# Kernel tuning notes

Hardware: AMD Instinct MI355X
Metric: run time of the kernel (lower is better)

## Reference

```python
import jax, jax.numpy as jnp
import numpy as np

NUM_CLASSES = 81
THRESH_HI = 0.5
THRESH_LO = 0.4
GAMMA = 2.0
ALPHA = 0.25
VARIANCE = (0.1, 0.2)  # cfg['variance'] in ssd.pytorch
B, P, T = 32, 24564, 20


def setup_inputs() -> dict:
    key = jax.random.key(0)
    k1, k2, k3, k4, k5, k6, k7 = jax.random.split(key, 7)
    loc_data = jax.random.normal(k1, (B, P, 4), jnp.float32)
    conf_data = jax.random.normal(k2, (B, P, NUM_CLASSES), jnp.float32)
    # priors in center form (cx, cy, w, h), all in [0,1]
    pcxy = jax.random.uniform(k3, (P, 2), minval=0.05, maxval=0.95)
    pwh = jax.random.uniform(k4, (P, 2), minval=0.04, maxval=0.5)
    priors = jnp.concatenate([pcxy, pwh], axis=-1).astype(jnp.float32)
    # ground-truth boxes in point form (xmin, ymin, xmax, ymax) + label
    tcxy = jax.random.uniform(k5, (B, T, 2), minval=0.1, maxval=0.9)
    twh = jax.random.uniform(k6, (B, T, 2), minval=0.05, maxval=0.4)
    boxes = jnp.clip(jnp.concatenate([tcxy - twh / 2, tcxy + twh / 2], -1), 0.0, 1.0)
    labels = jax.random.randint(k7, (B, T), 0, NUM_CLASSES - 1).astype(jnp.float32)
    targets = jnp.concatenate([boxes, labels[..., None]], axis=-1)  # [B,T,5]
    return {"loc_data": loc_data, "conf_data": conf_data, "priors": priors, "targets": targets}


def point_form(pr):
    # center form -> (xmin,ymin,xmax,ymax)
    return jnp.concatenate([pr[:, :2] - pr[:, 2:] / 2, pr[:, :2] + pr[:, 2:] / 2], -1)


def jaccard(box_a, box_b):
    # box_a [T,4], box_b [P,4], both point form -> IoU [T,P]
    lt = jnp.maximum(box_a[:, None, :2], box_b[None, :, :2])
    rb = jnp.minimum(box_a[:, None, 2:], box_b[None, :, 2:])
    wh = jnp.clip(rb - lt, 0.0)
    inter = wh[..., 0] * wh[..., 1]
    area_a = ((box_a[:, 2] - box_a[:, 0]) * (box_a[:, 3] - box_a[:, 1]))[:, None]
    area_b = ((box_b[:, 2] - box_b[:, 0]) * (box_b[:, 3] - box_b[:, 1]))[None, :]
    return inter / (area_a + area_b - inter)


def encode(matched, priors):
    # matched [P,4] point form, priors [P,4] center form
    g_cxcy = ((matched[:, :2] + matched[:, 2:]) / 2 - priors[:, :2]) / (VARIANCE[0] * priors[:, 2:])
    g_wh = jnp.log((matched[:, 2:] - matched[:, :2]) / priors[:, 2:]) / VARIANCE[1]
    return jnp.concatenate([g_cxcy, g_wh], -1)


def match_one(truths, labels, priors):
    # truths [T,4] point form, labels [T], priors [P,4] center form
    ov = jaccard(truths, point_form(priors))          # [T,P]
    best_prior_idx = jnp.argmax(ov, axis=1)           # [T] best prior per gt
    best_truth_overlap = jnp.max(ov, axis=0)          # [P]
    best_truth_idx = jnp.argmax(ov, axis=0)           # [P]
    # ensure every gt box keeps its best prior
    best_truth_overlap = best_truth_overlap.at[best_prior_idx].set(2.0)
    best_truth_idx = best_truth_idx.at[best_prior_idx].set(jnp.arange(truths.shape[0]))
    matched = truths[best_truth_idx]                  # [P,4]
    conf = labels[best_truth_idx].astype(jnp.int32) + 1
    conf = jnp.where(best_truth_overlap < THRESH_HI, -1, conf)  # ignore band
    conf = jnp.where(best_truth_overlap < THRESH_LO, 0, conf)   # background
    return encode(matched, priors), conf


def reference(loc_data, conf_data, priors, targets):
    truths = targets[..., :4]
    labels = targets[..., 4]
    loc_t, conf_t = jax.vmap(lambda t, l: match_one(t, l, priors))(truths, labels)
    pos = conf_t > 0                                  # [B,P]
    # smooth L1 over positive priors (sum reduction)
    diff = loc_data - loc_t
    ad = jnp.abs(diff)
    sl1 = jnp.where(ad < 1.0, 0.5 * diff * diff, ad - 0.5)
    loss_l = jnp.sum(sl1 * pos[..., None])
    # focal loss over ALL locations (ignore conf==-1)
    logits = conf_data.reshape(-1, NUM_CLASSES)
    tgt = conf_t.reshape(-1)
    valid = tgt >= 0
    tgt_safe = jnp.where(valid, tgt, 0)
    logpt = jnp.take_along_axis(jax.nn.log_softmax(logits, -1), tgt_safe[:, None], 1)[:, 0]
    pt = jnp.exp(logpt)
    alpha_t = jnp.where(tgt > 0, ALPHA, 1.0 - ALPHA)
    fl = -alpha_t * (1.0 - pt) ** GAMMA * logpt
    loss_c = jnp.sum(jnp.where(valid, fl, 0.0))
    n = jnp.sum(pos).astype(loc_data.dtype)
    return loss_l / n, loss_c / n
```

## Files before the change

### kernel.cpp

```cpp
#include <hip/hip_runtime.h>

#define NCLS 81
#define BB 32
#define PP 24564
#define TT 20
#define K3_BLOCKS 4096
#define K3_THREADS 256
#define KM_BLOCKS_X 96

__device__ __forceinline__ float iou_rn(float tx1, float ty1, float tx2, float ty2, float ta,
                                        float X1, float Y1, float X2, float Y2, float pa)
{
    float lx = fmaxf(tx1, X1);
    float ly = fmaxf(ty1, Y1);
    float rx = fminf(tx2, X2);
    float ry = fminf(ty2, Y2);
    float w = fmaxf(__fsub_rn(rx, lx), 0.0f);
    float h = fmaxf(__fsub_rn(ry, ly), 0.0f);
    float inter = __fmul_rn(w, h);
    float denom = __fsub_rn(__fadd_rn(ta, pa), inter);
    return __fdiv_rn(inter, denom);
}

__global__ __launch_bounds__(1024)
void k_best_prior(const float* __restrict__ priors,
                  const float* __restrict__ targets,
                  unsigned long long* __restrict__ bp)
{
    const int t = blockIdx.x;
    const int b = blockIdx.y;
    const float* tb = targets + (b * TT + t) * 5;
    const float tx1 = tb[0], ty1 = tb[1], tx2 = tb[2], ty2 = tb[3];
    const float ta = __fmul_rn(__fsub_rn(tx2, tx1), __fsub_rn(ty2, ty1));

    unsigned long long best = 0ull;
    for (int p = threadIdx.x; p < PP; p += 1024) {
        float px = priors[p * 4 + 0], py = priors[p * 4 + 1];
        float pw = priors[p * 4 + 2], ph = priors[p * 4 + 3];
        float hw = __fmul_rn(pw, 0.5f), hh = __fmul_rn(ph, 0.5f);
        float X1 = __fsub_rn(px, hw), Y1 = __fsub_rn(py, hh);
        float X2 = __fadd_rn(px, hw), Y2 = __fadd_rn(py, hh);
        float pa = __fmul_rn(__fsub_rn(X2, X1), __fsub_rn(Y2, Y1));
        float ov = iou_rn(tx1, ty1, tx2, ty2, ta, X1, Y1, X2, Y2, pa);
        unsigned long long pk = ((unsigned long long)__float_as_uint(ov) << 32)
                              | (unsigned long long)(0xFFFFFFFFu - (unsigned)p);
        if (pk > best) best = pk;
    }

    __shared__ unsigned long long red[1024];
    red[threadIdx.x] = best;
    __syncthreads();
    for (int s = 512; s > 0; s >>= 1) {
        if (threadIdx.x < s) {
            if (red[threadIdx.x + s] > red[threadIdx.x]) red[threadIdx.x] = red[threadIdx.x + s];
        }
        __syncthreads();
    }
    if (threadIdx.x == 0) bp[b * TT + t] = red[0];
}

__global__ __launch_bounds__(256)
void k_match(const float* __restrict__ loc,
             const float* __restrict__ priors,
             const float* __restrict__ targets,
             const unsigned long long* __restrict__ bp,
             unsigned char* __restrict__ code,
             float* __restrict__ pl, float* __restrict__ pn)
{
    const int b = blockIdx.y;
    const int p = blockIdx.x * 256 + threadIdx.x;

    __shared__ float trb[TT * 5];
    __shared__ unsigned int bpb[TT];
    if (threadIdx.x < TT * 5) trb[threadIdx.x] = targets[b * TT * 5 + threadIdx.x];
    if (threadIdx.x < TT)
        bpb[threadIdx.x] = 0xFFFFFFFFu - (unsigned)(bp[b * TT + threadIdx.x] & 0xFFFFFFFFull);
    __syncthreads();

    float accL = 0.0f, accN = 0.0f;

    if (p < PP) {
        float px = priors[p * 4 + 0], py = priors[p * 4 + 1];
        float pw = priors[p * 4 + 2], ph = priors[p * 4 + 3];
        float hw = __fmul_rn(pw, 0.5f), hh = __fmul_rn(ph, 0.5f);
        float X1 = __fsub_rn(px, hw), Y1 = __fsub_rn(py, hh);
        float X2 = __fadd_rn(px, hw), Y2 = __fadd_rn(py, hh);
        float pa = __fmul_rn(__fsub_rn(X2, X1), __fsub_rn(Y2, Y1));

        float bov = -1.0f;
        int bt = 0;
        #pragma unroll
        for (int t = 0; t < TT; ++t) {
            float tx1 = trb[t * 5 + 0], ty1 = trb[t * 5 + 1];
            float tx2 = trb[t * 5 + 2], ty2 = trb[t * 5 + 3];
            float ta2 = __fmul_rn(__fsub_rn(tx2, tx1), __fsub_rn(ty2, ty1));
            float ov = iou_rn(tx1, ty1, tx2, ty2, ta2, X1, Y1, X2, Y2, pa);
            if (ov > bov) { bov = ov; bt = t; }
        }
        bool forced = false;
        #pragma unroll
        for (int t = 0; t < TT; ++t) {
            if (bpb[t] == (unsigned)p) { bt = t; forced = true; }
        }
        if (forced) bov = 2.0f;

        int c = (int)trb[bt * 5 + 4] + 1;
        if (bov < 0.5f) c = -1;
        if (bov < 0.4f) c = 0;

        const int r = b * PP + p;
        code[r] = (unsigned char)(c + 1);

        if (c > 0) {
            float mx1 = trb[bt * 5 + 0], my1 = trb[bt * 5 + 1];
            float mx2 = trb[bt * 5 + 2], my2 = trb[bt * 5 + 3];
            float cx = __fmul_rn(__fadd_rn(mx1, mx2), 0.5f);
            float cy = __fmul_rn(__fadd_rn(my1, my2), 0.5f);
            float gx = __fdiv_rn(__fsub_rn(cx, px), __fmul_rn(0.1f, pw));
            float gy = __fdiv_rn(__fsub_rn(cy, py), __fmul_rn(0.1f, ph));
            float gw = __fdiv_rn(logf(__fdiv_rn(__fsub_rn(mx2, mx1), pw)), 0.2f);
            float gh = __fdiv_rn(logf(__fdiv_rn(__fsub_rn(my2, my1), ph)), 0.2f);
            const float* ld = loc + (size_t)r * 4;
            float g0 = ld[0] - gx, g1 = ld[1] - gy, g2 = ld[2] - gw, g3 = ld[3] - gh;
            float a0 = fabsf(g0), a1 = fabsf(g1), a2 = fabsf(g2), a3 = fabsf(g3);
            accL += (a0 < 1.0f) ? 0.5f * g0 * g0 : (a0 - 0.5f);
            accL += (a1 < 1.0f) ? 0.5f * g1 * g1 : (a1 - 0.5f);
            accL += (a2 < 1.0f) ? 0.5f * g2 * g2 : (a2 - 0.5f);
            accL += (a3 < 1.0f) ? 0.5f * g3 * g3 : (a3 - 0.5f);
            accN += 1.0f;
        }
    }

    __shared__ float red[256];
    red[threadIdx.x] = accL;
    __syncthreads();
    for (int s = 128; s; s >>= 1) {
        if (threadIdx.x < s) red[threadIdx.x] += red[threadIdx.x + s];
        __syncthreads();
    }
    if (threadIdx.x == 0) pl[blockIdx.y * KM_BLOCKS_X + blockIdx.x] = red[0];
    __syncthreads();

    red[threadIdx.x] = accN;
    __syncthreads();
    for (int s = 128; s; s >>= 1) {
        if (threadIdx.x < s) red[threadIdx.x] += red[threadIdx.x + s];
        __syncthreads();
    }
    if (threadIdx.x == 0) pn[blockIdx.y * KM_BLOCKS_X + blockIdx.x] = red[0];
}

__global__ __launch_bounds__(K3_THREADS)
void k_loss(const float* __restrict__ conf,
            const unsigned char* __restrict__ code,
            float* __restrict__ pc)
{
    const int lane = threadIdx.x & 15;
    const int gid = (blockIdx.x * K3_THREADS + threadIdx.x) >> 4;
    const int ngroups = (K3_BLOCKS * K3_THREADS) >> 4;

    float accC = 0.0f;

    for (int r = gid; r < BB * PP; r += ngroups) {
        const float* row = conf + (size_t)r * NCLS;

        float x0 = row[lane];
        float x1 = row[lane + 16];
        float x2 = row[lane + 32];
        float x3 = row[lane + 48];
        float x4 = row[lane + 64];
        int c = (int)code[r] - 1;

        float se = __expf(x0) + __expf(x1) + __expf(x2) + __expf(x3) + __expf(x4);
        if (lane == 0) se += __expf(row[80]);
        #pragma unroll
        for (int s = 8; s; s >>= 1) se += __shfl_xor(se, s, 16);

        if (lane == 0 && c >= 0) {
            float xt = row[c];
            float logpt = xt - __logf(se);
            float pt = __expf(logpt);
            float at = (c > 0) ? 0.25f : 0.75f;
            float om = 1.0f - pt;
            accC -= at * om * om * logpt;
        }
    }

    __shared__ float red[K3_THREADS];
    red[threadIdx.x] = accC;
    __syncthreads();
    for (int s = K3_THREADS / 2; s; s >>= 1) {
        if (threadIdx.x < s) red[threadIdx.x] += red[threadIdx.x + s];
        __syncthreads();
    }
    if (threadIdx.x == 0) pc[blockIdx.x] = red[0];
}

__global__ __launch_bounds__(256)
void k_final(const float* __restrict__ pl, const float* __restrict__ pn,
             const float* __restrict__ pc, float* __restrict__ out)
{
    __shared__ float sl[256], sc[256], sn[256];
    float L = 0.0f, C = 0.0f, N = 0.0f;
    for (int i = threadIdx.x; i < BB * KM_BLOCKS_X; i += 256) { L += pl[i]; N += pn[i]; }
    for (int i = threadIdx.x; i < K3_BLOCKS; i += 256) C += pc[i];
    sl[threadIdx.x] = L; sc[threadIdx.x] = C; sn[threadIdx.x] = N;
    __syncthreads();
    for (int s = 128; s; s >>= 1) {
        if (threadIdx.x < s) {
            sl[threadIdx.x] += sl[threadIdx.x + s];
            sc[threadIdx.x] += sc[threadIdx.x + s];
            sn[threadIdx.x] += sn[threadIdx.x + s];
        }
        __syncthreads();
    }
    if (threadIdx.x == 0) {
        out[0] = sl[0] / sn[0];
        out[1] = sc[0] / sn[0];
    }
}

extern "C" void kernel_launch(void* const* d_in, const int* in_sizes, int n_in,
                              void* d_out, int out_size, void* d_ws, size_t ws_size,
                              hipStream_t stream)
{
    const float* loc     = (const float*)d_in[0];
    const float* conf    = (const float*)d_in[1];
    const float* priors  = (const float*)d_in[2];
    const float* targets = (const float*)d_in[3];
    float* out = (float*)d_out;

    char* ws = (char*)d_ws;
    unsigned long long* bp = (unsigned long long*)ws;
    unsigned char* code = (unsigned char*)(ws + 4096);
    float* pl = (float*)(ws + 4096 + 790528);
    float* pn = pl + BB * KM_BLOCKS_X;
    float* pc = pn + BB * KM_BLOCKS_X;

    k_best_prior<<<dim3(TT, BB), 1024, 0, stream>>>(priors, targets, bp);
    k_match<<<dim3(KM_BLOCKS_X, BB), 256, 0, stream>>>(loc, priors, targets, bp, code, pl, pn);
    k_loss<<<K3_BLOCKS, K3_THREADS, 0, stream>>>(conf, code, pc);
    k_final<<<1, 256, 0, stream>>>(pl, pn, pc, out);
}
```

Baseline: 94.65 us.

## Stage logit rows through shared memory with vectorized loads in focal loss kernel

The focal-loss kernel now copies contiguous 128-row chunks of logits into shared memory using float4 loads, then lets two threads per row compute the softmax denominator from LDS. This replaces strided per-lane scalar global loads with fully vectorized coalesced transfers. The large shared buffer lowers occupancy and the load and compute phases are serialized within each block, with barriers in between.

```diff
diff --git a/kernel.cpp b/kernel.cpp
--- a/kernel.cpp
+++ b/kernel.cpp
@@ -4,9 +4,11 @@
 #define BB 32
 #define PP 24564
 #define TT 20
-#define K3_BLOCKS 4096
-#define K3_THREADS 256
 #define KM_BLOCKS_X 96
+#define KL_BLOCKS 2048
+#define KL_ROWS 128
+#define KL_CHUNKS ((BB * PP) / KL_ROWS)
+#define KL_F4 ((KL_ROWS * NCLS) / 4)
 
 __device__ __forceinline__ float iou_rn(float tx1, float ty1, float tx2, float ty2, float ta,
                                         float X1, float Y1, float X2, float Y2, float pa)
@@ -150,50 +152,58 @@
     if (threadIdx.x == 0) pn[blockIdx.y * KM_BLOCKS_X + blockIdx.x] = red[0];
 }
 
-__global__ __launch_bounds__(K3_THREADS)
+__global__ __launch_bounds__(256)
 void k_loss(const float* __restrict__ conf,
             const unsigned char* __restrict__ code,
             float* __restrict__ pc)
 {
-    const int lane = threadIdx.x & 15;
-    const int gid = (blockIdx.x * K3_THREADS + threadIdx.x) >> 4;
-    const int ngroups = (K3_BLOCKS * K3_THREADS) >> 4;
+    __shared__ float buf[KL_ROWS * NCLS];
+
+    const int tid = threadIdx.x;
+    const int rl = tid >> 1;
+    const int half = tid & 1;
+    const int base = half ? 41 : 0;
 
     float accC = 0.0f;
 
-    for (int r = gid; r < BB * PP; r += ngroups) {
-        const float* row = conf + (size_t)r * NCLS;
-
-        float x0 = row[lane];
-        float x1 = row[lane + 16];
-        float x2 = row[lane + 32];
-        float x3 = row[lane + 48];
-        float x4 = row[lane + 64];
-        int c = (int)code[r] - 1;
-
-        float se = __expf(x0) + __expf(x1) + __expf(x2) + __expf(x3) + __expf(x4);
-        if (lane == 0) se += __expf(row[80]);
+    for (int chunk = blockIdx.x; chunk < KL_CHUNKS; chunk += KL_BLOCKS) {
+        const float4* src = (const float4*)conf + (size_t)chunk * KL_F4;
+        float4* dst = (float4*)buf;
         #pragma unroll
-        for (int s = 8; s; s >>= 1) se += __shfl_xor(se, s, 16);
-
-        if (lane == 0 && c >= 0) {
-            float xt = row[c];
-            float logpt = xt - __logf(se);
-            float pt = __expf(logpt);
-            float at = (c > 0) ? 0.25f : 0.75f;
-            float om = 1.0f - pt;
-            accC -= at * om * om * logpt;
-        }
-    }
-
-    __shared__ float red[K3_THREADS];
-    red[threadIdx.x] = accC;
-    __syncthreads();
-    for (int s = K3_THREADS / 2; s; s >>= 1) {
-        if (threadIdx.x < s) red[threadIdx.x] += red[threadIdx.x + s];
-        __syncthreads();
-    }
-    if (threadIdx.x == 0) pc[blockIdx.x] = red[0];
+        for (int i = 0; i < 10; ++i) dst[tid + i * 256] = src[tid + i * 256];
+        if (tid < KL_F4 - 2560) dst[2560 + tid] = src[2560 + tid];
+        __syncthreads();
+
+        const float* row = buf + rl * NCLS;
+        float se = 0.0f;
+        #pragma unroll 8
+        for (int i = 0; i < 40; ++i) se += __expf(row[base + i]);
+        if (!half) se += __expf(row[40]);
+        se += __shfl_xor(se, 1);
+
+        if (!half) {
+            int r = chunk * KL_ROWS + rl;
+            int c = (int)code[r] - 1;
+            if (c >= 0) {
+                float xt = row[c];
+                float logpt = xt - __logf(se);
+                float pt = __expf(logpt);
+                float at = (c > 0) ? 0.25f : 0.75f;
+                float om = 1.0f - pt;
+                accC -= at * om * om * logpt;
+            }
+        }
+        __syncthreads();
+    }
+
+    __shared__ float red[256];
+    red[tid] = accC;
+    __syncthreads();
+    for (int s = 128; s; s >>= 1) {
+        if (tid < s) red[tid] += red[tid + s];
+        __syncthreads();
+    }
+    if (tid == 0) pc[blockIdx.x] = red[0];
 }
 
 __global__ __launch_bounds__(256)
@@ -203,7 +213,7 @@
     __shared__ float sl[256], sc[256], sn[256];
     float L = 0.0f, C = 0.0f, N = 0.0f;
     for (int i = threadIdx.x; i < BB * KM_BLOCKS_X; i += 256) { L += pl[i]; N += pn[i]; }
-    for (int i = threadIdx.x; i < K3_BLOCKS; i += 256) C += pc[i];
+    for (int i = threadIdx.x; i < KL_BLOCKS; i += 256) C += pc[i];
     sl[threadIdx.x] = L; sc[threadIdx.x] = C; sn[threadIdx.x] = N;
     __syncthreads();
     for (int s = 128; s; s >>= 1) {
@@ -239,6 +249,6 @@
 
     k_best_prior<<<dim3(TT, BB), 1024, 0, stream>>>(priors, targets, bp);
     k_match<<<dim3(KM_BLOCKS_X, BB), 256, 0, stream>>>(loc, priors, targets, bp, code, pl, pn);
-    k_loss<<<K3_BLOCKS, K3_THREADS, 0, stream>>>(conf, code, pc);
+    k_loss<<<KL_BLOCKS, 256, 0, stream>>>(conf, code, pc);
     k_final<<<1, 256, 0, stream>>>(pl, pn, pc, out);
 }
```

New measurement: 86.69 us. -8.4%, faster.
